# Kernel optimization log

Measured on AMD Instinct MI355X. Metric: run time of the kernel, lower is better.

Reference implementation:

```python
import jax, jax.numpy as jnp
import numpy as np

C = 256
RED = 8
CK = C // RED  # 32


def setup_inputs() -> dict:
    key = jax.random.key(0)
    ks = jax.random.split(key, 7)
    x = jax.random.normal(ks[0], (4, C, 64, 64), dtype=jnp.float32)
    s = 1.0 / np.sqrt(C)
    key_W = jax.random.uniform(ks[1], (CK, C), minval=-s, maxval=s, dtype=jnp.float32)
    key_b = jax.random.uniform(ks[2], (CK,), minval=-s, maxval=s, dtype=jnp.float32)
    query_W = jax.random.uniform(ks[3], (CK, C), minval=-s, maxval=s, dtype=jnp.float32)
    query_b = jax.random.uniform(ks[4], (CK,), minval=-s, maxval=s, dtype=jnp.float32)
    value_W = jax.random.uniform(ks[5], (C, C), minval=-s, maxval=s, dtype=jnp.float32)
    value_b = jax.random.uniform(ks[6], (C,), minval=-s, maxval=s, dtype=jnp.float32)
    alpha = jnp.zeros((1,), dtype=jnp.float32)
    return {"x": x, "key_W": key_W, "key_b": key_b, "query_W": query_W,
            "query_b": query_b, "value_W": value_W, "value_b": value_b,
            "alpha": alpha}


def reference(x, key_W, key_b, query_W, query_b, value_W, value_b, alpha):
    B, Cc, H, W = x.shape
    N = H * W
    xf = x.reshape(B, Cc, N)  # [B, C, N]
    # 1x1 convs == per-pixel linear projections
    k = jnp.einsum('kc,bcn->bkn', key_W, xf) + key_b[None, :, None]     # [B, CK, N]
    q = jnp.einsum('kc,bcn->bkn', query_W, xf) + query_b[None, :, None]  # [B, CK, N]
    v = jnp.einsum('oc,bcn->bon', value_W, xf) + value_b[None, :, None]  # [B, C, N]
    # energy[b, i, j] = key_i . query_j
    energy = jnp.einsum('bki,bkj->bij', k, q)  # [B, N, N]
    attn = jax.nn.softmax(energy, axis=-1)
    # out[b, c, i] = sum_j v[b, c, j] * attn[b, i, j]
    out = jnp.einsum('bcj,bij->bci', v, attn)  # [B, C, N]
    out = out.reshape(B, Cc, H, W)
    return alpha * out + x
```

## Files before the change

kernel.cpp:

```cpp
#include <hip/hip_runtime.h>

#define C_DIM 256
#define CK_DIM 32
#define NPIX 4096
#define BATCH 4

typedef __attribute__((ext_vector_type(8))) short bf16x8;
typedef __attribute__((ext_vector_type(4))) float f32x4;
typedef __attribute__((ext_vector_type(16))) float f32x16;
typedef __attribute__((ext_vector_type(4))) unsigned short us4;

__device__ __forceinline__ unsigned short f2bf(float f) {
    union { float f; unsigned int u; } c; c.f = f;
    unsigned int r = c.u + 0x7FFFu + ((c.u >> 16) & 1u);
    return (unsigned short)(r >> 16);
}

__global__ __launch_bounds__(256) void wprep_kernel(
    const float* __restrict__ kW, const float* __restrict__ qW,
    const float* __restrict__ vW, unsigned short* __restrict__ wbf)
{
    int i4 = (blockIdx.x * 256 + threadIdx.x) * 4;
    int o = i4 >> 8, c = i4 & 255;
    const float* src = (o < 32) ? kW + o * 256 + c
                     : (o < 64) ? qW + (o - 32) * 256 + c
                                : vW + (o - 64) * 256 + c;
    float4 f = *(const float4*)src;
    us4 p; p.x = f2bf(f.x); p.y = f2bf(f.y); p.z = f2bf(f.z); p.w = f2bf(f.w);
    *(us4*)&wbf[i4] = p;
}

#define XP 264
__global__ __launch_bounds__(256) void proj_kernel(
    const float* __restrict__ x,
    const unsigned short* __restrict__ wbf,
    const float* __restrict__ key_b, const float* __restrict__ query_b,
    const float* __restrict__ value_b,
    unsigned short* __restrict__ kT,
    unsigned short* __restrict__ qT,
    unsigned short* __restrict__ vt)
{
    const int b  = blockIdx.y;
    const int n0 = blockIdx.x * 32;
    const int t  = threadIdx.x;
    const int w    = t >> 6;
    const int lane = t & 63;
    const int mrow = lane & 15;
    const int quad = lane >> 4;
    const int oh   = w >> 1;
    const int ns   = (w & 1) * 16;

    __shared__ __align__(16) unsigned short smem[14592];
    #define XT(n, c)       smem[(n) * XP + (c)]
    #define VS(nsb, c, nn) smem[(nsb) * 6144 + (c) * 24 + (nn)]
    #define KQS(n, o)      smem[12288 + (n) * 72 + (o)]

    const float* xb = x + (size_t)b * C_DIM * NPIX + n0;
    const int cb = (t >> 3) * 4;
    const int n4 = (t & 7) * 4;
    #pragma unroll
    for (int it = 0; it < 2; ++it) {
        int c0 = it * 128 + cb;
        float4 r0 = *(const float4*)(xb + (size_t)(c0 + 0) * NPIX + n4);
        float4 r1 = *(const float4*)(xb + (size_t)(c0 + 1) * NPIX + n4);
        float4 r2 = *(const float4*)(xb + (size_t)(c0 + 2) * NPIX + n4);
        float4 r3 = *(const float4*)(xb + (size_t)(c0 + 3) * NPIX + n4);
        float d0[4] = {r0.x, r0.y, r0.z, r0.w};
        float d1[4] = {r1.x, r1.y, r1.z, r1.w};
        float d2[4] = {r2.x, r2.y, r2.z, r2.w};
        float d3[4] = {r3.x, r3.y, r3.z, r3.w};
        #pragma unroll
        for (int d = 0; d < 4; ++d) {
            us4 p; p.x = f2bf(d0[d]); p.y = f2bf(d1[d]);
                   p.z = f2bf(d2[d]); p.w = f2bf(d3[d]);
            *(us4*)&XT(n4 + d, c0) = p;
        }
    }
    __syncthreads();

    f32x4 acc[10];
    #pragma unroll
    for (int ot = 0; ot < 10; ++ot) acc[ot] = (f32x4){0.f, 0.f, 0.f, 0.f};
    const int obase = oh * 160;

    #pragma unroll 2
    for (int ck = 0; ck < 256; ck += 32) {
        bf16x8 bx = *(const bf16x8*)&XT(ns + mrow, ck + quad * 8);
        #pragma unroll
        for (int ot = 0; ot < 10; ++ot) {
            bf16x8 aw = *(const bf16x8*)(wbf + (size_t)(obase + ot * 16 + mrow) * 256
                                         + ck + quad * 8);
            acc[ot] = __builtin_amdgcn_mfma_f32_16x16x32_bf16(aw, bx, acc[ot], 0, 0, 0);
        }
    }
    __syncthreads();

    #pragma unroll
    for (int ot = 0; ot < 10; ++ot) {
        #pragma unroll
        for (int r = 0; r < 4; ++r) {
            int o = obase + 16 * ot + 4 * quad + r;
            float bias = (o < 32) ? key_b[o] : (o < 64) ? query_b[o - 32] : value_b[o - 64];
            unsigned short val = f2bf(acc[ot][r] + bias);
            if (o < 64) KQS(ns + mrow, o) = val;
            else        VS(ns >> 4, o - 64, mrow) = val;
        }
    }
    __syncthreads();

    {
        int n = t >> 3, o4 = (t & 7) * 4;
        *(us4*)&kT[((size_t)b * NPIX + n0 + n) * CK_DIM + o4] = *(const us4*)&KQS(n, o4);
        *(us4*)&qT[((size_t)b * NPIX + n0 + n) * CK_DIM + o4] = *(const us4*)&KQS(n, 32 + o4);
    }
    #pragma unroll
    for (int it = 0; it < 8; ++it) {
        int flat = it * 256 + t;
        int nsb = flat >> 10, c = (flat >> 2) & 255, nn = (flat & 3) * 4;
        unsigned short* vbase = vt + ((size_t)b * (NPIX / 16) + n0 / 16 + nsb) * (C_DIM * 16);
        *(us4*)&vbase[c * 16 + nn] = *(const us4*)&VS(nsb, c, nn);
    }
    #undef XT
    #undef VS
    #undef KQS
}

__global__ __launch_bounds__(256) void attn_kernel(
    const unsigned short* __restrict__ kT,
    const unsigned short* __restrict__ qT,
    const unsigned short* __restrict__ vt,
    const float* __restrict__ x, const float* __restrict__ alpha,
    float* __restrict__ out)
{
    const int f  = blockIdx.x;
    const int b  = (f & 7) >> 1;
    const int i0 = (((f >> 3) << 1) | (f & 1)) * 64;
    const int t  = threadIdx.x;
    const int w    = t >> 6;
    const int lane = t & 63;
    const int mrow = lane & 15;
    const int quad = lane >> 4;
    const int m32  = lane & 31;
    const int half = lane >> 5;
    const int c0   = w * 64;

    __shared__ __align__(16) unsigned short Pt[2][64][136];
    __shared__ float lred[4][64];

    const unsigned short* kTb = kT + (size_t)b * NPIX * CK_DIM;
    const unsigned short* qTb = qT + (size_t)b * NPIX * CK_DIM;
    const unsigned short* vtb = vt + (size_t)b * (NPIX / 16) * (C_DIM * 16);

    bf16x8 kf[4];
    #pragma unroll
    for (int is = 0; is < 4; ++is)
        kf[is] = *(const bf16x8*)(kTb + (size_t)(i0 + 16 * is + mrow) * CK_DIM + quad * 8);

    f32x16 acc[2][2];
    #pragma unroll
    for (int cs = 0; cs < 2; ++cs)
        #pragma unroll
        for (int ih = 0; ih < 2; ++ih)
            #pragma unroll
            for (int r = 0; r < 16; ++r) acc[cs][ih][r] = 0.0f;

    float lacc[4] = {0.f, 0.f, 0.f, 0.f};
    int pp = 0;

    for (int jt = 0; jt < NPIX; jt += 128) {
        bf16x8 av[8][2];
        #pragma unroll
        for (int jb = 0; jb < 8; ++jb) {
            const unsigned short* vp = vtb + (size_t)(jt / 16 + jb) * (C_DIM * 16)
                                       + (size_t)(c0 + m32) * 16 + half * 8;
            av[jb][0] = *(const bf16x8*)vp;
            av[jb][1] = *(const bf16x8*)(vp + 32 * 16);
        }

        int jw = jt + 32 * w;
        #pragma unroll
        for (int js = 0; js < 2; ++js) {
            bf16x8 aq = *(const bf16x8*)(qTb + (size_t)(jw + 16 * js + mrow) * CK_DIM + quad * 8);
            #pragma unroll
            for (int is = 0; is < 4; ++is) {
                f32x4 d = __builtin_amdgcn_mfma_f32_16x16x32_bf16(
                    aq, kf[is], (f32x4){0.f, 0.f, 0.f, 0.f}, 0, 0, 0);
                float p0 = __expf(d[0]), p1 = __expf(d[1]);
                float p2 = __expf(d[2]), p3 = __expf(d[3]);
                lacc[is] += (p0 + p1) + (p2 + p3);
                us4 p;
                p.x = f2bf(p0); p.y = f2bf(p1); p.z = f2bf(p2); p.w = f2bf(p3);
                *(us4*)&Pt[pp][16 * is + mrow][32 * w + 16 * js + 4 * quad] = p;
            }
        }
        __syncthreads();

        #pragma unroll
        for (int jb = 0; jb < 8; ++jb) {
            bf16x8 bp0 = *(const bf16x8*)&Pt[pp][m32][16 * jb + half * 8];
            bf16x8 bp1 = *(const bf16x8*)&Pt[pp][32 + m32][16 * jb + half * 8];
            acc[0][0] = __builtin_amdgcn_mfma_f32_32x32x16_bf16(av[jb][0], bp0, acc[0][0], 0, 0, 0);
            acc[1][0] = __builtin_amdgcn_mfma_f32_32x32x16_bf16(av[jb][1], bp0, acc[1][0], 0, 0, 0);
            acc[0][1] = __builtin_amdgcn_mfma_f32_32x32x16_bf16(av[jb][0], bp1, acc[0][1], 0, 0, 0);
            acc[1][1] = __builtin_amdgcn_mfma_f32_32x32x16_bf16(av[jb][1], bp1, acc[1][1], 0, 0, 0);
        }
        pp ^= 1;
    }

    #pragma unroll
    for (int is = 0; is < 4; ++is) {
        lacc[is] += __shfl_xor(lacc[is], 16);
        lacc[is] += __shfl_xor(lacc[is], 32);
    }
    if (lane < 16) {
        #pragma unroll
        for (int is = 0; is < 4; ++is) lred[w][16 * is + lane] = lacc[is];
    }
    __syncthreads();

    const float al = alpha[0];
    float rs[2];
    #pragma unroll
    for (int ih = 0; ih < 2; ++ih) {
        int li = 32 * ih + m32;
        float l = (lred[0][li] + lred[1][li]) + (lred[2][li] + lred[3][li]);
        rs[ih] = al / l;
    }

    const float* xb = x + (size_t)b * C_DIM * NPIX;
    float* ob = out + (size_t)b * C_DIM * NPIX;
    #pragma unroll
    for (int cs = 0; cs < 2; ++cs)
        #pragma unroll
        for (int ih = 0; ih < 2; ++ih) {
            int i = i0 + 32 * ih + m32;
            #pragma unroll
            for (int r = 0; r < 16; ++r) {
                int c = c0 + 32 * cs + (r & 3) + 8 * (r >> 2) + 4 * half;
                size_t idx = (size_t)c * NPIX + i;
                ob[idx] = acc[cs][ih][r] * rs[ih] + xb[idx];
            }
        }
}

extern "C" void kernel_launch(void* const* d_in, const int* in_sizes, int n_in,
                              void* d_out, int out_size, void* d_ws, size_t ws_size,
                              hipStream_t stream) {
    const float* x       = (const float*)d_in[0];
    const float* key_W   = (const float*)d_in[1];
    const float* key_b   = (const float*)d_in[2];
    const float* query_W = (const float*)d_in[3];
    const float* query_b = (const float*)d_in[4];
    const float* value_W = (const float*)d_in[5];
    const float* value_b = (const float*)d_in[6];
    const float* alpha   = (const float*)d_in[7];
    float* out = (float*)d_out;

    unsigned short* kT  = (unsigned short*)d_ws;
    unsigned short* qT  = kT + (size_t)BATCH * NPIX * CK_DIM;
    unsigned short* vt  = qT + (size_t)BATCH * NPIX * CK_DIM;
    unsigned short* wbf = vt + (size_t)BATCH * C_DIM * NPIX;

    wprep_kernel<<<80, 256, 0, stream>>>(key_W, query_W, value_W, wbf);

    dim3 gridA(NPIX / 32, BATCH);
    proj_kernel<<<gridA, 256, 0, stream>>>(x, wbf, key_b, query_b, value_b, kT, qT, vt);

    attn_kernel<<<256, 256, 0, stream>>>(kT, qT, vt, x, alpha, out);
}
```

Baseline: 162.4 us.

## Warp-specialize attention into producer and consumer warps, prefetch projection weights

```diff
diff --git a/kernel.cpp b/kernel.cpp
--- a/kernel.cpp
+++ b/kernel.cpp
@@ -82,16 +82,26 @@
     #pragma unroll
     for (int ot = 0; ot < 10; ++ot) acc[ot] = (f32x4){0.f, 0.f, 0.f, 0.f};
     const int obase = oh * 160;
-
-    #pragma unroll 2
+    const unsigned short* wp = wbf + (size_t)(obase + mrow) * 256 + quad * 8;
+
+    bf16x8 awc[10], awn[10];
+    #pragma unroll
+    for (int ot = 0; ot < 10; ++ot)
+        awc[ot] = *(const bf16x8*)(wp + (size_t)ot * 16 * 256);
+
+    #pragma unroll
     for (int ck = 0; ck < 256; ck += 32) {
         bf16x8 bx = *(const bf16x8*)&XT(ns + mrow, ck + quad * 8);
-        #pragma unroll
-        for (int ot = 0; ot < 10; ++ot) {
-            bf16x8 aw = *(const bf16x8*)(wbf + (size_t)(obase + ot * 16 + mrow) * 256
-                                         + ck + quad * 8);
-            acc[ot] = __builtin_amdgcn_mfma_f32_16x16x32_bf16(aw, bx, acc[ot], 0, 0, 0);
-        }
+        if (ck < 224) {
+            #pragma unroll
+            for (int ot = 0; ot < 10; ++ot)
+                awn[ot] = *(const bf16x8*)(wp + (size_t)ot * 16 * 256 + ck + 32);
+        }
+        #pragma unroll
+        for (int ot = 0; ot < 10; ++ot)
+            acc[ot] = __builtin_amdgcn_mfma_f32_16x16x32_bf16(awc[ot], bx, acc[ot], 0, 0, 0);
+        #pragma unroll
+        for (int ot = 0; ot < 10; ++ot) awc[ot] = awn[ot];
     }
     __syncthreads();
 
@@ -125,7 +135,7 @@
     #undef KQS
 }
 
-__global__ __launch_bounds__(256) void attn_kernel(
+__global__ __launch_bounds__(512) void attn_kernel(
     const unsigned short* __restrict__ kT,
     const unsigned short* __restrict__ qT,
     const unsigned short* __restrict__ vt,
@@ -134,7 +144,7 @@
 {
     const int f  = blockIdx.x;
     const int b  = (f & 7) >> 1;
-    const int i0 = (((f >> 3) << 1) | (f & 1)) * 64;
+    const int i0 = ((f >> 3) * 2 + (f & 1)) * 64;
     const int t  = threadIdx.x;
     const int w    = t >> 6;
     const int lane = t & 63;
@@ -142,7 +152,6 @@
     const int quad = lane >> 4;
     const int m32  = lane & 31;
     const int half = lane >> 5;
-    const int c0   = w * 64;
 
     __shared__ __align__(16) unsigned short Pt[2][64][136];
     __shared__ float lred[4][64];
@@ -151,36 +160,20 @@
     const unsigned short* qTb = qT + (size_t)b * NPIX * CK_DIM;
     const unsigned short* vtb = vt + (size_t)b * (NPIX / 16) * (C_DIM * 16);
 
-    bf16x8 kf[4];
-    #pragma unroll
-    for (int is = 0; is < 4; ++is)
-        kf[is] = *(const bf16x8*)(kTb + (size_t)(i0 + 16 * is + mrow) * CK_DIM + quad * 8);
-
-    f32x16 acc[2][2];
-    #pragma unroll
-    for (int cs = 0; cs < 2; ++cs)
-        #pragma unroll
-        for (int ih = 0; ih < 2; ++ih)
-            #pragma unroll
-            for (int r = 0; r < 16; ++r) acc[cs][ih][r] = 0.0f;
-
-    float lacc[4] = {0.f, 0.f, 0.f, 0.f};
     int pp = 0;
 
-    for (int jt = 0; jt < NPIX; jt += 128) {
-        bf16x8 av[8][2];
-        #pragma unroll
-        for (int jb = 0; jb < 8; ++jb) {
-            const unsigned short* vp = vtb + (size_t)(jt / 16 + jb) * (C_DIM * 16)
-                                       + (size_t)(c0 + m32) * 16 + half * 8;
-            av[jb][0] = *(const bf16x8*)vp;
-            av[jb][1] = *(const bf16x8*)(vp + 32 * 16);
-        }
-
-        int jw = jt + 32 * w;
+    if (w < 4) {
+        const int pw = w;
+        bf16x8 kf[4];
+        #pragma unroll
+        for (int is = 0; is < 4; ++is)
+            kf[is] = *(const bf16x8*)(kTb + (size_t)(i0 + 16 * is + mrow) * CK_DIM + quad * 8);
+
+        float lacc[4] = {0.f, 0.f, 0.f, 0.f};
+
         #pragma unroll
         for (int js = 0; js < 2; ++js) {
-            bf16x8 aq = *(const bf16x8*)(qTb + (size_t)(jw + 16 * js + mrow) * CK_DIM + quad * 8);
+            bf16x8 aq = *(const bf16x8*)(qTb + (size_t)(32 * pw + 16 * js + mrow) * CK_DIM + quad * 8);
             #pragma unroll
             for (int is = 0; is < 4; ++is) {
                 f32x4 d = __builtin_amdgcn_mfma_f32_16x16x32_bf16(
@@ -188,59 +181,123 @@
                 float p0 = __expf(d[0]), p1 = __expf(d[1]);
                 float p2 = __expf(d[2]), p3 = __expf(d[3]);
                 lacc[is] += (p0 + p1) + (p2 + p3);
-                us4 p;
-                p.x = f2bf(p0); p.y = f2bf(p1); p.z = f2bf(p2); p.w = f2bf(p3);
-                *(us4*)&Pt[pp][16 * is + mrow][32 * w + 16 * js + 4 * quad] = p;
-            }
-        }
+                us4 p; p.x = f2bf(p0); p.y = f2bf(p1); p.z = f2bf(p2); p.w = f2bf(p3);
+                *(us4*)&Pt[0][16 * is + mrow][32 * pw + 16 * js + 4 * quad] = p;
+            }
+        }
+        bf16x8 aqc[2];
+        #pragma unroll
+        for (int js = 0; js < 2; ++js)
+            aqc[js] = *(const bf16x8*)(qTb + (size_t)(128 + 32 * pw + 16 * js + mrow) * CK_DIM + quad * 8);
+
         __syncthreads();
 
+        for (int jt = 0; jt < NPIX; jt += 128) {
+            bf16x8 aqn[2];
+            int jpre = (jt + 256) & (NPIX - 1);
+            #pragma unroll
+            for (int js = 0; js < 2; ++js)
+                aqn[js] = *(const bf16x8*)(qTb + (size_t)(jpre + 32 * pw + 16 * js + mrow) * CK_DIM + quad * 8);
+
+            if (jt + 128 < NPIX) {
+                #pragma unroll
+                for (int js = 0; js < 2; ++js) {
+                    #pragma unroll
+                    for (int is = 0; is < 4; ++is) {
+                        f32x4 d = __builtin_amdgcn_mfma_f32_16x16x32_bf16(
+                            aqc[js], kf[is], (f32x4){0.f, 0.f, 0.f, 0.f}, 0, 0, 0);
+                        float p0 = __expf(d[0]), p1 = __expf(d[1]);
+                        float p2 = __expf(d[2]), p3 = __expf(d[3]);
+                        lacc[is] += (p0 + p1) + (p2 + p3);
+                        us4 p; p.x = f2bf(p0); p.y = f2bf(p1); p.z = f2bf(p2); p.w = f2bf(p3);
+                        *(us4*)&Pt[pp ^ 1][16 * is + mrow][32 * pw + 16 * js + 4 * quad] = p;
+                    }
+                }
+            }
+            aqc[0] = aqn[0]; aqc[1] = aqn[1];
+            __syncthreads();
+            pp ^= 1;
+        }
+
+        #pragma unroll
+        for (int is = 0; is < 4; ++is) {
+            lacc[is] += __shfl_xor(lacc[is], 16);
+            lacc[is] += __shfl_xor(lacc[is], 32);
+        }
+        if (lane < 16) {
+            #pragma unroll
+            for (int is = 0; is < 4; ++is) lred[pw][16 * is + lane] = lacc[is];
+        }
+        __syncthreads();
+    } else {
+        const int cw = w - 4;
+        const int c0 = cw * 64;
+
+        f32x16 acc[2][2];
+        #pragma unroll
+        for (int cs = 0; cs < 2; ++cs)
+            #pragma unroll
+            for (int ih = 0; ih < 2; ++ih)
+                #pragma unroll
+                for (int r = 0; r < 16; ++r) acc[cs][ih][r] = 0.0f;
+
+        bf16x8 av[8][2];
         #pragma unroll
         for (int jb = 0; jb < 8; ++jb) {
-            bf16x8 bp0 = *(const bf16x8*)&Pt[pp][m32][16 * jb + half * 8];
-            bf16x8 bp1 = *(const bf16x8*)&Pt[pp][32 + m32][16 * jb + half * 8];
-            acc[0][0] = __builtin_amdgcn_mfma_f32_32x32x16_bf16(av[jb][0], bp0, acc[0][0], 0, 0, 0);
-            acc[1][0] = __builtin_amdgcn_mfma_f32_32x32x16_bf16(av[jb][1], bp0, acc[1][0], 0, 0, 0);
-            acc[0][1] = __builtin_amdgcn_mfma_f32_32x32x16_bf16(av[jb][0], bp1, acc[0][1], 0, 0, 0);
-            acc[1][1] = __builtin_amdgcn_mfma_f32_32x32x16_bf16(av[jb][1], bp1, acc[1][1], 0, 0, 0);
-        }
-        pp ^= 1;
-    }
-
-    #pragma unroll
-    for (int is = 0; is < 4; ++is) {
-        lacc[is] += __shfl_xor(lacc[is], 16);
-        lacc[is] += __shfl_xor(lacc[is], 32);
-    }
-    if (lane < 16) {
-        #pragma unroll
-        for (int is = 0; is < 4; ++is) lred[w][16 * is + lane] = lacc[is];
-    }
-    __syncthreads();
-
-    const float al = alpha[0];
-    float rs[2];
-    #pragma unroll
-    for (int ih = 0; ih < 2; ++ih) {
-        int li = 32 * ih + m32;
-        float l = (lred[0][li] + lred[1][li]) + (lred[2][li] + lred[3][li]);
-        rs[ih] = al / l;
-    }
-
-    const float* xb = x + (size_t)b * C_DIM * NPIX;
-    float* ob = out + (size_t)b * C_DIM * NPIX;
-    #pragma unroll
-    for (int cs = 0; cs < 2; ++cs)
+            const unsigned short* vp = vtb + (size_t)jb * (C_DIM * 16)
+                                       + (size_t)(c0 + m32) * 16 + half * 8;
+            av[jb][0] = *(const bf16x8*)vp;
+            av[jb][1] = *(const bf16x8*)(vp + 32 * 16);
+        }
+        __syncthreads();
+
+        for (int jt = 0; jt < NPIX; jt += 128) {
+            #pragma unroll
+            for (int jb = 0; jb < 8; ++jb) {
+                bf16x8 bp0 = *(const bf16x8*)&Pt[pp][m32][16 * jb + half * 8];
+                bf16x8 bp1 = *(const bf16x8*)&Pt[pp][32 + m32][16 * jb + half * 8];
+                acc[0][0] = __builtin_amdgcn_mfma_f32_32x32x16_bf16(av[jb][0], bp0, acc[0][0], 0, 0, 0);
+                acc[1][0] = __builtin_amdgcn_mfma_f32_32x32x16_bf16(av[jb][1], bp0, acc[1][0], 0, 0, 0);
+                acc[0][1] = __builtin_amdgcn_mfma_f32_32x32x16_bf16(av[jb][0], bp1, acc[0][1], 0, 0, 0);
+                acc[1][1] = __builtin_amdgcn_mfma_f32_32x32x16_bf16(av[jb][1], bp1, acc[1][1], 0, 0, 0);
+            }
+            int jpre = (jt + 128) & (NPIX - 1);
+            #pragma unroll
+            for (int jb = 0; jb < 8; ++jb) {
+                const unsigned short* vp = vtb + (size_t)(jpre / 16 + jb) * (C_DIM * 16)
+                                           + (size_t)(c0 + m32) * 16 + half * 8;
+                av[jb][0] = *(const bf16x8*)vp;
+                av[jb][1] = *(const bf16x8*)(vp + 32 * 16);
+            }
+            __syncthreads();
+            pp ^= 1;
+        }
+        __syncthreads();
+
+        const float al = alpha[0];
+        float rs[2];
         #pragma unroll
         for (int ih = 0; ih < 2; ++ih) {
-            int i = i0 + 32 * ih + m32;
-            #pragma unroll
-            for (int r = 0; r < 16; ++r) {
-                int c = c0 + 32 * cs + (r & 3) + 8 * (r >> 2) + 4 * half;
-                size_t idx = (size_t)c * NPIX + i;
-                ob[idx] = acc[cs][ih][r] * rs[ih] + xb[idx];
-            }
-        }
+            int li = 32 * ih + m32;
+            float l = (lred[0][li] + lred[1][li]) + (lred[2][li] + lred[3][li]);
+            rs[ih] = al / l;
+        }
+
+        const float* xb = x + (size_t)b * C_DIM * NPIX;
+        float* ob = out + (size_t)b * C_DIM * NPIX;
+        #pragma unroll
+        for (int cs = 0; cs < 2; ++cs)
+            #pragma unroll
+            for (int ih = 0; ih < 2; ++ih) {
+                int i = i0 + 32 * ih + m32;
+                #pragma unroll
+                for (int r = 0; r < 16; ++r) {
+                    int c = c0 + 32 * cs + (r & 3) + 8 * (r >> 2) + 4 * half;
+                    size_t idx = (size_t)c * NPIX + i;
+                    ob[idx] = acc[cs][ih][r] * rs[ih] + xb[idx];
+                }
+            }
+    }
 }
 
 extern "C" void kernel_launch(void* const* d_in, const int* in_sizes, int n_in,
@@ -266,5 +323,5 @@
     dim3 gridA(NPIX / 32, BATCH);
     proj_kernel<<<gridA, 256, 0, stream>>>(x, wbf, key_b, query_b, value_b, kT, qT, vt);
 
-    attn_kernel<<<256, 256, 0, stream>>>(kT, qT, vt, x, alpha, out);
-}
+    attn_kernel<<<256, 512, 0, stream>>>(kT, qT, vt, x, alpha, out);
+}
```

New measurement: 150.6 us. 7.3% less time.
